# Performance work log

Hardware: AMD Instinct MI355X
Metric: run time of the kernel (lower is better)

The kernel has to match this reference:

```python
import jax, jax.numpy as jnp
import numpy as np

B, N, C = 4, 4096, 512
C8 = C // 8

def setup_inputs() -> dict:
    key = jax.random.key(0)
    ks = jax.random.split(key, 4)
    x = jax.random.normal(ks[0], (B, N, C), dtype=jnp.float32)
    # 1x1 Conv1D kernels == dense matmuls over channel dim
    Wf = jax.random.normal(ks[1], (C, C8), dtype=jnp.float32) * 0.02
    bf = jnp.zeros((C8,), dtype=jnp.float32)
    Wg = jax.random.normal(ks[2], (C, C8), dtype=jnp.float32) * 0.02
    bg = jnp.zeros((C8,), dtype=jnp.float32)
    Wh = jax.random.normal(ks[3], (C, C), dtype=jnp.float32) * 0.02
    bh = jnp.zeros((C,), dtype=jnp.float32)
    gamma = jnp.float32(1.0)  # learned scalar (zero-init in original; nonzero to exercise path)
    return {"x": x, "Wf": Wf, "bf": bf, "Wg": Wg, "bg": bg, "Wh": Wh, "bh": bh, "gamma": gamma}

def reference(x, Wf, bf, Wg, bg, Wh, bh, gamma):
    # 1x1 conv projections (kernel_size=1 -> per-position matmul)
    f_x = jnp.einsum('bnc,cd->bnd', x, Wf) + bf          # [B, N, C/8]
    g_x = jnp.einsum('bnc,cd->bnd', x, Wg) + bg          # [B, N, C/8]
    h_x = jnp.einsum('bnc,cd->bnd', x, Wh) + bh          # [B, N, C]
    # unscaled single-head attention: softmax(f g^T) h
    scores = jnp.einsum('bnd,bmd->bnm', f_x, g_x)        # [B, N, N]
    attn = jax.nn.softmax(scores, axis=-1)
    out = jnp.einsum('bnm,bmd->bnd', attn, h_x)          # [B, N, C]
    return x + gamma * out
```

## Files before the change

### kernel.cpp

```cpp
#include <hip/hip_runtime.h>
#include <stdint.h>

typedef uint16_t u16;
typedef __attribute__((ext_vector_type(8)))  __bf16    bf16x8;
typedef __attribute__((ext_vector_type(4)))  __bf16    bf16x4;
typedef __attribute__((ext_vector_type(8)))  uint16_t  u16x8;
typedef __attribute__((ext_vector_type(4)))  uint16_t  u16x4;
typedef __attribute__((ext_vector_type(4)))  float     f32x4;

#define LOG2E 1.44269504088896340736f
#define MFMA16(a, b, c) __builtin_amdgcn_mfma_f32_16x16x32_bf16((a), (b), (c), 0, 0, 0)

__device__ __forceinline__ u16 f2b(float f) {
  uint32_t u = __builtin_bit_cast(uint32_t, f);
  u += 0x7fffu + ((u >> 16) & 1u);
  return (u16)(u >> 16);
}

__device__ __forceinline__ bf16x8 ldsFrag(const u16* base, int row, int chunk) {
  const u16* p = base + row * 64 + ((chunk ^ (row & 7)) << 3);
  u16x8 raw = *(const u16x8*)p;
  return __builtin_bit_cast(bf16x8, raw);
}

__device__ __forceinline__ void dma16(const u16* g, u16* l) {
  __builtin_amdgcn_global_load_lds(
      (const __attribute__((address_space(1))) uint32_t*)g,
      (__attribute__((address_space(3))) uint32_t*)l, 16, 0, 0);
}

__global__ __launch_bounds__(256) void xpack(
    const float* __restrict__ x, u16* __restrict__ xb,
    const float* __restrict__ Wf, const float* __restrict__ Wg,
    const float* __restrict__ Wh, const float* __restrict__ bfv,
    const float* __restrict__ bgv, const float* __restrict__ bhv,
    u16* __restrict__ Wt, float* __restrict__ biasc) {
  __shared__ u16 T[64 * 64];
  const int t = threadIdx.x;
  if (blockIdx.x < 4096) {
    size_t idx = ((size_t)blockIdx.x * 256 + t) * 8;
    f32x4 a0 = *(const f32x4*)(x + idx);
    f32x4 a1 = *(const f32x4*)(x + idx + 4);
    u16x8 v;
#pragma unroll
    for (int i = 0; i < 4; ++i) { v[i] = f2b(a0[i]); v[4 + i] = f2b(a1[i]); }
    *(u16x8*)(xb + idx) = v;
    return;
  }
  const int bid = blockIdx.x - 4096;
  const int nt = bid >> 3;
  const int kt = bid & 7;
  const int n0 = nt * 64, k0 = kt * 64;
  const float* src; int stride, cbase; float scale = 1.0f;
  if (nt == 0)      { src = Wf; stride = 64;  cbase = 0;        scale = LOG2E; }
  else if (nt == 1) { src = Wg; stride = 64;  cbase = 0; }
  else              { src = Wh; stride = 512; cbase = n0 - 128; }
  const int cl = (t & 15) * 4, r0 = t >> 4;
#pragma unroll
  for (int j = 0; j < 4; ++j) {
    int r = r0 + j * 16;
    f32x4 v = *(const f32x4*)(src + (size_t)(k0 + r) * stride + cbase + cl);
    u16x4 o;
#pragma unroll
    for (int i = 0; i < 4; ++i) o[i] = f2b(v[i] * scale);
    *(u16x4*)(T + r * 64 + cl) = o;
  }
  __syncthreads();
  const int n = t >> 2, kq = (t & 3) * 16;
  u16x8 a, b2;
#pragma unroll
  for (int i = 0; i < 8; ++i) { a[i] = T[(kq + i) * 64 + n]; b2[i] = T[(kq + 8 + i) * 64 + n]; }
  *(u16x8*)(Wt + (size_t)(n0 + n) * 512 + k0 + kq) = a;
  *(u16x8*)(Wt + (size_t)(n0 + n) * 512 + k0 + kq + 8) = b2;
  if (kt == 0 && t < 64) {
    float bv = (nt == 0) ? bfv[t] * LOG2E : (nt == 1) ? bgv[t] : bhv[cbase + t];
    biasc[n0 + t] = bv;
  }
}

__global__ __launch_bounds__(256, 4) void proj_gemm(
    const u16* __restrict__ xb, const u16* __restrict__ Wt,
    const float* __restrict__ biasc,
    u16* __restrict__ fo, u16* __restrict__ go, u16* __restrict__ ht) {
  __shared__ u16 smem[128 * 64 + 64 * 64];
  u16* lds_a = smem;
  u16* lds_b = smem + 128 * 64;
  const int t = threadIdx.x, lane = t & 63, wave = t >> 6;
  const int m0 = blockIdx.x * 128, n0 = blockIdx.y * 64;
  const int wr = wave >> 1, wc = wave & 1;
  const int l15 = lane & 15, l4 = lane >> 4;
  const int dmarow = lane >> 3, dmachunk = (lane & 7) ^ (lane >> 3);

  f32x4 acc[4][2];
#pragma unroll
  for (int i = 0; i < 4; ++i)
#pragma unroll
    for (int j = 0; j < 2; ++j) acc[i][j] = (f32x4)(0.f);

  for (int kb = 0; kb < 8; ++kb) {
    const int k0 = kb * 64;
    if (kb) __syncthreads();
#pragma unroll
    for (int ii = 0; ii < 4; ++ii) {
      int rw = wave * 32 + ii * 8;
      dma16(xb + (size_t)(m0 + rw + dmarow) * 512 + k0 + dmachunk * 8,
            lds_a + rw * 64);
    }
#pragma unroll
    for (int ii = 0; ii < 2; ++ii) {
      int rw = wave * 16 + ii * 8;
      dma16(Wt + (size_t)(n0 + rw + dmarow) * 512 + k0 + dmachunk * 8,
            lds_b + rw * 64);
    }
    __syncthreads();
#pragma unroll
    for (int ks = 0; ks < 2; ++ks) {
      const int chunk = ks * 4 + l4;
      bf16x8 af[4], bq[2];
#pragma unroll
      for (int mt = 0; mt < 4; ++mt) af[mt] = ldsFrag(lds_a, wr * 64 + mt * 16 + l15, chunk);
#pragma unroll
      for (int nt = 0; nt < 2; ++nt) bq[nt] = ldsFrag(lds_b, wc * 32 + nt * 16 + l15, chunk);
#pragma unroll
      for (int mt = 0; mt < 4; ++mt)
#pragma unroll
        for (int nt = 0; nt < 2; ++nt) acc[mt][nt] = MFMA16(af[mt], bq[nt], acc[mt][nt]);
    }
  }

  if (n0 >= 128) {
    __syncthreads();
#pragma unroll
    for (int nt = 0; nt < 2; ++nt) {
      int nl = wc * 32 + nt * 16 + l15;
      float bv = biasc[n0 + nl];
#pragma unroll
      for (int mt = 0; mt < 4; ++mt) {
        int mb = wr * 64 + mt * 16 + (l4 << 2);
        f32x4 a = acc[mt][nt];
        u16x4 v;
#pragma unroll
        for (int r = 0; r < 4; ++r) v[r] = f2b(a[r] + bv);
        u16* dst = smem + nl * 128 + (((mb >> 3) ^ (nl & 7)) << 3) + (mb & 7);
        *(u16x4*)dst = v;
      }
    }
    __syncthreads();
    const int bb = m0 >> 12, posb = m0 & 4095;
    const int row0 = t >> 4, c16 = t & 15;
#pragma unroll
    for (int j = 0; j < 4; ++j) {
      int rr = row0 + j * 16;
      u16x8 v = *(const u16x8*)(smem + rr * 128 + ((c16 ^ (rr & 7)) << 3));
      int vcol = n0 - 128 + rr;
      *(u16x8*)(ht + ((size_t)(bb * 512 + vcol) << 12) + posb + c16 * 8) = v;
    }
  } else {
#pragma unroll
    for (int nt = 0; nt < 2; ++nt) {
      int n = wc * 32 + nt * 16 + l15;
      float bv = biasc[n0 + n];
#pragma unroll
      for (int mt = 0; mt < 4; ++mt) {
        int mrow = m0 + wr * 64 + mt * 16 + (l4 << 2);
        f32x4 a = acc[mt][nt];
        if (n0 == 0) {
#pragma unroll
          for (int r = 0; r < 4; ++r) fo[(size_t)(mrow + r) * 64 + n] = f2b(a[r] + bv);
        } else {
#pragma unroll
          for (int r = 0; r < 4; ++r) go[(size_t)(mrow + r) * 64 + n] = f2b(a[r] + bv);
        }
      }
    }
  }
}

__global__ __launch_bounds__(512, 4) void attn12(
    const u16* __restrict__ fq, const u16* __restrict__ gk,
    const u16* __restrict__ ht, const float* __restrict__ x,
    const float* __restrict__ gamma_p, float* __restrict__ out) {
  __shared__ u16 lds_g[64 * 64];
  __shared__ u16 lds_p[128 * 64];
  __shared__ float lds_red[8 * 64];
  __shared__ float lds_linv[128];

  const int i = blockIdx.x;
  const int slice = i & 15;
  const int b = slice >> 2, vq = slice & 3;
  const int qb = i >> 4;
  const int q0 = qb * 128, vc0 = vq * 128;

  const int t = threadIdx.x, lane = t & 63, w = t >> 6;
  const int l15 = lane & 15, l4 = lane >> 4;
  const int h = w >> 2, kq = w & 3;
  const float gamma = gamma_p[0];
  const int dmarow = lane >> 3, dmachunk = (lane & 7) ^ (lane >> 3);

  const u16* gkb = gk + (size_t)(b * 4096) * 64;
  const u16* htw = ht + ((size_t)(b * 512 + vc0 + w * 16)) * 4096;

  bf16x8 fB[4][2];
#pragma unroll
  for (int qt = 0; qt < 4; ++qt)
#pragma unroll
    for (int ks = 0; ks < 2; ++ks) {
      const u16* p = fq + (size_t)(b * 4096 + q0 + h * 64 + qt * 16 + l15) * 64 + ks * 32 + l4 * 8;
      fB[qt][ks] = __builtin_bit_cast(bf16x8, *(const u16x8*)p);
    }

  f32x4 oacc[8];
#pragma unroll
  for (int qt = 0; qt < 8; ++qt) oacc[qt] = (f32x4)(0.f);
  float lrun[4] = {0.f, 0.f, 0.f, 0.f};

  auto stage_g = [&](int k0g) {
    const u16* src = gkb + (size_t)(k0g + w * 8 + dmarow) * 64 + dmachunk * 8;
    dma16(src, lds_g + (w * 8) * 64);
  };

  stage_g(0);
  __syncthreads();

  for (int kt = 0; kt < 64; ++kt) {
    const int k0 = kt * 64;
    f32x4 sacc[4];
#pragma unroll
    for (int qt = 0; qt < 4; ++qt) sacc[qt] = (f32x4)(0.f);
#pragma unroll
    for (int ks = 0; ks < 2; ++ks) {
      bf16x8 gA = ldsFrag(lds_g, kq * 16 + l15, ks * 4 + l4);
#pragma unroll
      for (int qt = 0; qt < 4; ++qt) sacc[qt] = MFMA16(gA, fB[qt][ks], sacc[qt]);
    }
#pragma unroll
    for (int qt = 0; qt < 4; ++qt) {
      f32x4 s = sacc[qt];
      f32x4 p;
#pragma unroll
      for (int r = 0; r < 4; ++r) p[r] = __builtin_amdgcn_exp2f(s[r]);
      lrun[qt] += (p[0] + p[1]) + (p[2] + p[3]);
      bf16x4 pb;
#pragma unroll
      for (int r = 0; r < 4; ++r) pb[r] = (__bf16)p[r];
      int row = h * 64 + qt * 16 + l15;
      int keyb = kq * 16 + (l4 << 2);
      u16* dst = lds_p + row * 64 + (((keyb >> 3) ^ (row & 7)) << 3) + (keyb & 7);
      *(u16x4*)dst = __builtin_bit_cast(u16x4, pb);
    }
    __syncthreads();
    if (kt < 63) stage_g(k0 + 64);
#pragma unroll
    for (int ks = 0; ks < 2; ++ks) {
      const u16* hp = htw + (size_t)l15 * 4096 + k0 + ks * 32 + l4 * 8;
      bf16x8 hb = __builtin_bit_cast(bf16x8, *(const u16x8*)hp);
#pragma unroll
      for (int qt = 0; qt < 8; ++qt) {
        bf16x8 pf = ldsFrag(lds_p, qt * 16 + l15, ks * 4 + l4);
        oacc[qt] = MFMA16(pf, hb, oacc[qt]);
      }
    }
    __syncthreads();
  }

#pragma unroll
  for (int qt = 0; qt < 4; ++qt) {
    lrun[qt] += __shfl_xor(lrun[qt], 16);
    lrun[qt] += __shfl_xor(lrun[qt], 32);
  }
  if (l4 == 0) {
#pragma unroll
    for (int qt = 0; qt < 4; ++qt) lds_red[w * 64 + qt * 16 + l15] = lrun[qt];
  }
  __syncthreads();
  if (t < 128) {
    int hh = t >> 6, ql = t & 63;
    float s = (lds_red[(hh * 4 + 0) * 64 + ql] + lds_red[(hh * 4 + 1) * 64 + ql]) +
              (lds_red[(hh * 4 + 2) * 64 + ql] + lds_red[(hh * 4 + 3) * 64 + ql]);
    lds_linv[t] = 1.0f / s;
  }
  __syncthreads();

#pragma unroll
  for (int qt = 0; qt < 8; ++qt) {
    f32x4 linv = *(const f32x4*)&lds_linv[qt * 16 + (l4 << 2)];
    int c = vc0 + w * 16 + l15;
#pragma unroll
    for (int r = 0; r < 4; ++r) {
      int q = q0 + qt * 16 + (l4 << 2) + r;
      size_t idx = ((size_t)(b * 4096 + q) << 9) + c;
      out[idx] = x[idx] + gamma * oacc[qt][r] * linv[r];
    }
  }
}

extern "C" void kernel_launch(void* const* d_in, const int* in_sizes, int n_in,
                              void* d_out, int out_size, void* d_ws, size_t ws_size,
                              hipStream_t stream) {
  const float* x   = (const float*)d_in[0];
  const float* Wf  = (const float*)d_in[1];
  const float* bfv = (const float*)d_in[2];
  const float* Wg  = (const float*)d_in[3];
  const float* bgv = (const float*)d_in[4];
  const float* Wh  = (const float*)d_in[5];
  const float* bhv = (const float*)d_in[6];
  const float* gam = (const float*)d_in[7];
  float* out = (float*)d_out;

  char* ws = (char*)d_ws;
  u16*   Wt    = (u16*)(ws);
  float* biasc = (float*)(ws + 655360);
  u16*   fo    = (u16*)(ws + 657920);
  u16*   go    = (u16*)(ws + 2755072);
  u16*   ht    = (u16*)(ws + 4852224);
  u16*   xb    = (u16*)(ws + 21629440);

  xpack<<<4176, 256, 0, stream>>>(x, xb, Wf, Wg, Wh, bfv, bgv, bhv, Wt, biasc);
  proj_gemm<<<dim3(128, 10), 256, 0, stream>>>(xb, Wt, biasc, fo, go, ht);
  attn12<<<512, 512, 0, stream>>>(fo, go, ht, x, gam, out);
}
```

Baseline: 218.0 us.

## Software-pipeline attention loop with double-buffered G and P tiles

Double-buffers the key tile and the probability tile in LDS so that the P·H MFMA for the previous key block runs in the same phase as the score computation for the current block. This cuts the two barriers per iteration down to one and issues the next G DMA and the H global loads earlier. In exchange it doubles LDS use (about 48KB per block), which may lower occupancy below the four blocks the launch bounds target, and it needs an epilogue for the last block.

```diff
diff --git a/kernel.cpp b/kernel.cpp
--- a/kernel.cpp
+++ b/kernel.cpp
@@ -176,12 +176,12 @@
   }
 }
 
-__global__ __launch_bounds__(512, 4) void attn12(
+__global__ __launch_bounds__(512, 4) void attn14(
     const u16* __restrict__ fq, const u16* __restrict__ gk,
     const u16* __restrict__ ht, const float* __restrict__ x,
     const float* __restrict__ gamma_p, float* __restrict__ out) {
-  __shared__ u16 lds_g[64 * 64];
-  __shared__ u16 lds_p[128 * 64];
+  __shared__ u16 lds_g[2][64 * 64];
+  __shared__ u16 lds_p[2][128 * 64];
   __shared__ float lds_red[8 * 64];
   __shared__ float lds_linv[128];
 
@@ -214,22 +214,32 @@
   for (int qt = 0; qt < 8; ++qt) oacc[qt] = (f32x4)(0.f);
   float lrun[4] = {0.f, 0.f, 0.f, 0.f};
 
-  auto stage_g = [&](int k0g) {
+  auto stage_g = [&](int k0g, u16* dst) {
     const u16* src = gkb + (size_t)(k0g + w * 8 + dmarow) * 64 + dmachunk * 8;
-    dma16(src, lds_g + (w * 8) * 64);
+    dma16(src, dst + (w * 8) * 64);
   };
 
-  stage_g(0);
+  stage_g(0, lds_g[0]);
   __syncthreads();
 
   for (int kt = 0; kt < 64; ++kt) {
     const int k0 = kt * 64;
+    const int cur = kt & 1;
+    if (kt < 63) stage_g(k0 + 64, lds_g[cur ^ 1]);
+
+    u16x8 hb0, hb1;
+    if (kt > 0) {
+      const int kp = k0 - 64;
+      hb0 = *(const u16x8*)(htw + (size_t)l15 * 4096 + kp + l4 * 8);
+      hb1 = *(const u16x8*)(htw + (size_t)l15 * 4096 + kp + 32 + l4 * 8);
+    }
+
     f32x4 sacc[4];
 #pragma unroll
     for (int qt = 0; qt < 4; ++qt) sacc[qt] = (f32x4)(0.f);
 #pragma unroll
     for (int ks = 0; ks < 2; ++ks) {
-      bf16x8 gA = ldsFrag(lds_g, kq * 16 + l15, ks * 4 + l4);
+      bf16x8 gA = ldsFrag(lds_g[cur], kq * 16 + l15, ks * 4 + l4);
 #pragma unroll
       for (int qt = 0; qt < 4; ++qt) sacc[qt] = MFMA16(gA, fB[qt][ks], sacc[qt]);
     }
@@ -245,22 +255,45 @@
       for (int r = 0; r < 4; ++r) pb[r] = (__bf16)p[r];
       int row = h * 64 + qt * 16 + l15;
       int keyb = kq * 16 + (l4 << 2);
-      u16* dst = lds_p + row * 64 + (((keyb >> 3) ^ (row & 7)) << 3) + (keyb & 7);
+      u16* dst = lds_p[cur] + row * 64 + (((keyb >> 3) ^ (row & 7)) << 3) + (keyb & 7);
       *(u16x4*)dst = __builtin_bit_cast(u16x4, pb);
     }
+
+    if (kt > 0) {
+      const u16* pprev = lds_p[cur ^ 1];
+      bf16x8 hbb0 = __builtin_bit_cast(bf16x8, hb0);
+      bf16x8 hbb1 = __builtin_bit_cast(bf16x8, hb1);
+#pragma unroll
+      for (int qt = 0; qt < 8; ++qt) {
+        bf16x8 pf0 = ldsFrag(pprev, qt * 16 + l15, l4);
+        oacc[qt] = MFMA16(pf0, hbb0, oacc[qt]);
+      }
+#pragma unroll
+      for (int qt = 0; qt < 8; ++qt) {
+        bf16x8 pf1 = ldsFrag(pprev, qt * 16 + l15, 4 + l4);
+        oacc[qt] = MFMA16(pf1, hbb1, oacc[qt]);
+      }
+    }
     __syncthreads();
-    if (kt < 63) stage_g(k0 + 64);
-#pragma unroll
-    for (int ks = 0; ks < 2; ++ks) {
-      const u16* hp = htw + (size_t)l15 * 4096 + k0 + ks * 32 + l4 * 8;
-      bf16x8 hb = __builtin_bit_cast(bf16x8, *(const u16x8*)hp);
-#pragma unroll
-      for (int qt = 0; qt < 8; ++qt) {
-        bf16x8 pf = ldsFrag(lds_p, qt * 16 + l15, ks * 4 + l4);
-        oacc[qt] = MFMA16(pf, hb, oacc[qt]);
-      }
-    }
-    __syncthreads();
+  }
+
+  {
+    const int kp = 63 * 64;
+    u16x8 h0 = *(const u16x8*)(htw + (size_t)l15 * 4096 + kp + l4 * 8);
+    u16x8 h1 = *(const u16x8*)(htw + (size_t)l15 * 4096 + kp + 32 + l4 * 8);
+    bf16x8 hbb0 = __builtin_bit_cast(bf16x8, h0);
+    bf16x8 hbb1 = __builtin_bit_cast(bf16x8, h1);
+    const u16* pprev = lds_p[1];
+#pragma unroll
+    for (int qt = 0; qt < 8; ++qt) {
+      bf16x8 pf0 = ldsFrag(pprev, qt * 16 + l15, l4);
+      oacc[qt] = MFMA16(pf0, hbb0, oacc[qt]);
+    }
+#pragma unroll
+    for (int qt = 0; qt < 8; ++qt) {
+      bf16x8 pf1 = ldsFrag(pprev, qt * 16 + l15, 4 + l4);
+      oacc[qt] = MFMA16(pf1, hbb1, oacc[qt]);
+    }
   }
 
 #pragma unroll
@@ -317,5 +350,5 @@
 
   xpack<<<4176, 256, 0, stream>>>(x, xb, Wf, Wg, Wh, bfv, bgv, bhv, Wt, biasc);
   proj_gemm<<<dim3(128, 10), 256, 0, stream>>>(xb, Wt, biasc, fo, go, ht);
-  attn12<<<512, 512, 0, stream>>>(fo, go, ht, x, gam, out);
-}
+  attn14<<<512, 512, 0, stream>>>(fo, go, ht, x, gam, out);
+}
```

Result: no change. 219.9 us (+0.9%).
